# Optimization experiments

Hardware: AMD Instinct MI355X
Metric: run time of the kernel (lower is better)

Reference implementation:

```python
import jax, jax.numpy as jnp
import numpy as np

H = 768
NH = 12
DH = H // NH  # 64


def setup_inputs() -> dict:
    key = jax.random.key(0)
    ks = jax.random.split(key, 20)
    s = 1.0 / np.sqrt(H)
    def lin(k, din, dout):
        kw, kb = jax.random.split(k)
        W = jax.random.uniform(kw, (din, dout), jnp.float32, -s, s)
        b = jax.random.uniform(kb, (dout,), jnp.float32, -s, s)
        return W, b
    Wq, bq = lin(ks[0], H, H)
    Wk, bk = lin(ks[1], H, H)
    Wv, bv = lin(ks[2], H, H)
    Wt, bt = lin(ks[3], H, H)
    Wi, bi = lin(ks[4], H, H)
    W1, b1 = lin(ks[5], H, H)
    W2, b2 = lin(ks[6], H, 1)
    text = jax.random.normal(ks[7], (8, 64, H), jnp.float32)
    image = jax.random.normal(ks[8], (8, 197, H), jnp.float32)
    return dict(text=text, image=image, Wq=Wq, bq=bq, Wk=Wk, bk=bk, Wv=Wv, bv=bv,
                Wt=Wt, bt=bt, Wi=Wi, bi=bi, W1=W1, b1=b1, W2=W2, b2=b2)


def reference(text, image, Wq, bq, Wk, bk, Wv, bv, Wt, bt, Wi, bi, W1, b1, W2, b2):
    bsz, t_len, _ = text.shape
    i_len = image.shape[1]
    # relevance gate MLP on broadcast product
    text_emb = text @ Wt + bt          # [b, t, H]
    image_emb = image @ Wi + bi        # [b, i, H]
    rel = text_emb[:, :, None, :] * image_emb[:, None, :, :]  # [b, t, i, H]
    rel = jax.nn.relu(rel @ W1 + b1)
    gate = jax.nn.sigmoid(rel @ W2 + b2)  # [b, t, i, 1]
    gate = gate.reshape(bsz, 1, t_len, i_len)
    # cross-attention
    def heads(x, L):
        return x.reshape(bsz, L, NH, DH).transpose(0, 2, 1, 3)  # [b, h, L, dh]
    q = heads(text @ Wq + bq, t_len)
    k = heads(image @ Wk + bk, i_len)
    v = heads(image @ Wv + bv, i_len)
    scores = jnp.einsum('bhtd,bhid->bhti', q, k) / np.sqrt(DH)
    probs = jax.nn.softmax(scores, axis=-1) * gate   # [b, h, t, i]
    ctx = jnp.einsum('bhti,bhid->bhtd', probs, v)    # [b, h, t, dh]
    return ctx.transpose(0, 2, 1, 3).reshape(bsz, t_len, H)
```

## Files before the change

kernel.cpp:

```cpp
#include <hip/hip_runtime.h>
#include <stdint.h>

#define HD 768
#define NHEADS 12
#define DHEAD 64
#define BATCH 8
#define TLEN 64
#define ILEN 197
#define NPAIRS 100864
#define MTILES 394

typedef __attribute__((ext_vector_type(8))) short short8;
typedef __attribute__((ext_vector_type(4))) float f32x4;

__device__ __forceinline__ short f2bf(float x) {
    union { float f; uint32_t u; } v; v.f = x;
    uint32_t r = v.u + 0x7FFFu + ((v.u >> 16) & 1u);
    return (short)(r >> 16);
}
__device__ __forceinline__ float bf2f(short s) {
    union { uint32_t u; float f; } v; v.u = ((uint32_t)(unsigned short)s) << 16;
    return v.f;
}
__device__ __forceinline__ void gll16(const void* g, void* l) {
    __builtin_amdgcn_global_load_lds(
        (const __attribute__((address_space(1))) unsigned int*)g,
        (__attribute__((address_space(3))) unsigned int*)l, 16, 0, 0);
}

__global__ __launch_bounds__(256) void prep_weights(
    const float* __restrict__ Wq, const float* __restrict__ Wk,
    const float* __restrict__ Wv, const float* __restrict__ Wt,
    const float* __restrict__ Wi, const float* __restrict__ W1,
    short* __restrict__ W5s, short* __restrict__ W1Bs)
{
    __shared__ float tile[64][65];
    int bx = blockIdx.x;
    int tid = threadIdx.x;
    if (bx >= 720) {
        int idx = bx - 720;
        int pn = idx / 12, kt = idx - pn * 12;
        int c = tid;
        int j = pn * 256 + c;
        char* dst = (char*)W1Bs + (size_t)idx * 32768 + c * 128;
        int swz = (c & 7) << 4;
#pragma unroll
        for (int kg = 0; kg < 8; ++kg) {
            short8 o;
#pragma unroll
            for (int e = 0; e < 8; ++e)
                o[e] = f2bf(W1[(size_t)(kt * 64 + kg * 8 + e) * HD + j]);
            *(short8*)(dst + ((kg * 16) ^ swz)) = o;
        }
        return;
    }
    int seg = bx / 144, ti = bx - seg * 144;
    const float* src = (seg == 0) ? Wt : (seg == 1) ? Wq : (seg == 2) ? Wi
                     : (seg == 3) ? Wk : Wv;
    int kt = ti / 12, ntile = ti - kt * 12;
#pragma unroll
    for (int pass = 0; pass < 16; ++pass) {
        int idx = pass * 256 + tid;
        int kk = idx >> 6, nn = idx & 63;
        tile[kk][nn] = src[(size_t)(kt * 64 + kk) * HD + ntile * 64 + nn];
    }
    __syncthreads();
    size_t base = ((size_t)(seg * 12 + ntile) * 12 + kt) * 8192;
#pragma unroll
    for (int pass = 0; pass < 16; ++pass) {
        int idx = pass * 256 + tid;
        int col = idx >> 6, kloc = idx & 63;
        float x = tile[kloc][col];
        short h = f2bf(x);
        short lw = f2bf(x - bf2f(h));
        int sidx = (col * 64 + kloc) ^ ((col & 7) << 3);
        W5s[base + sidx] = h;
        W5s[base + 4096 + sidx] = lw;
    }
}

__global__ __launch_bounds__(256, 1) void proj_kernel(
    const float* __restrict__ X, int M,
    const short* __restrict__ W5s, int segbase,
    const float* __restrict__ bias0, const float* __restrict__ bias1,
    const float* __restrict__ bias2,
    float* __restrict__ out0, float* __restrict__ out1, float* __restrict__ out2)
{
    __shared__ __align__(16) short Bs[2][8192];
    int tid = threadIdx.x;
    int l = tid & 63, w = tid >> 6;
    int lo = l & 15, grp = l >> 4;
    int y = blockIdx.y;
    int segl = y / 12, ntile = y - segl * 12;
    int seg = segbase + segl;
    const char* wsrc = (const char*)W5s + (size_t)((seg * 12 + ntile) * 12) * 16384;
    {
        const char* s = wsrc + w * 4096 + l * 16;
        char* d = (char*)&Bs[0][0] + w * 4096;
        gll16(s, d); gll16(s + 1024, d + 1024);
        gll16(s + 2048, d + 2048); gll16(s + 3072, d + 3072);
    }
    int arow = blockIdx.x * 64 + w * 16 + lo;
    bool aok = arow < M;
    const float* xrow = X + (size_t)(aok ? arow : 0) * HD;
    short8 ah[24], al[24];
#pragma unroll
    for (int kc = 0; kc < 24; ++kc) {
        int kb = kc * 32 + grp * 8;
        float4 xa = {0.f, 0.f, 0.f, 0.f}, xb = {0.f, 0.f, 0.f, 0.f};
        if (aok) { xa = *(const float4*)(xrow + kb); xb = *(const float4*)(xrow + kb + 4); }
        float xs[8] = {xa.x, xa.y, xa.z, xa.w, xb.x, xb.y, xb.z, xb.w};
#pragma unroll
        for (int e = 0; e < 8; ++e) {
            short hh = f2bf(xs[e]);
            ah[kc][e] = hh;
            al[kc][e] = f2bf(xs[e] - bf2f(hh));
        }
    }
    __syncthreads();

    f32x4 acc[4];
    f32x4 z4 = {0.f, 0.f, 0.f, 0.f};
#pragma unroll
    for (int js = 0; js < 4; ++js) acc[js] = z4;

#pragma unroll
    for (int kk = 0; kk < 12; ++kk) {
        const short* buf = &Bs[kk & 1][0];
        if (kk < 11) {
            const char* s = wsrc + (size_t)(kk + 1) * 16384 + w * 4096 + l * 16;
            char* d = (char*)&Bs[(kk + 1) & 1][0] + w * 4096;
            gll16(s, d); gll16(s + 1024, d + 1024);
            gll16(s + 2048, d + 2048); gll16(s + 3072, d + 3072);
            asm volatile("s_waitcnt vmcnt(4)" ::: "memory");
        } else {
            asm volatile("s_waitcnt vmcnt(0)" ::: "memory");
        }
        __builtin_amdgcn_s_barrier();
        asm volatile("" ::: "memory");
#pragma unroll
        for (int js = 0; js < 4; ++js) {
            int col = js * 16 + lo;
            int base = col * 64;
            int sw = (col & 7) << 3;
#pragma unroll
            for (int kcl = 0; kcl < 2; ++kcl) {
                int idx = (base + kcl * 32 + grp * 8) ^ sw;
                short8 bh = *(const short8*)&buf[idx];
                short8 bl = *(const short8*)&buf[4096 + idx];
                int kc = kk * 2 + kcl;
                acc[js] = __builtin_amdgcn_mfma_f32_16x16x32_bf16(ah[kc], bh, acc[js], 0, 0, 0);
                acc[js] = __builtin_amdgcn_mfma_f32_16x16x32_bf16(ah[kc], bl, acc[js], 0, 0, 0);
                acc[js] = __builtin_amdgcn_mfma_f32_16x16x32_bf16(al[kc], bh, acc[js], 0, 0, 0);
            }
        }
        asm volatile("s_waitcnt lgkmcnt(0)" ::: "memory");
        __builtin_amdgcn_s_barrier();
        asm volatile("" ::: "memory");
    }
    const float* bp = (segl == 0) ? bias0 : (segl == 1) ? bias1 : bias2;
    float* op = (segl == 0) ? out0 : (segl == 1) ? out1 : out2;
#pragma unroll
    for (int js = 0; js < 4; ++js) {
        int cc = ntile * 64 + js * 16 + lo;
        float bvv = bp[cc];
#pragma unroll
        for (int r = 0; r < 4; ++r) {
            int orow = blockIdx.x * 64 + w * 16 + grp * 4 + r;
            if (orow < M) op[(size_t)orow * HD + cc] = acc[js][r] + bvv;
        }
    }
}

__global__ __launch_bounds__(256) void build_a(
    const float* __restrict__ te, const float* __restrict__ ie,
    short* __restrict__ As, int mstart)
{
    int bx = blockIdx.x;
    int m_l = bx / 12, kt = bx - m_l * 12;
    int tid = threadIdx.x;
    int p = (mstart + m_l) * 256 + tid;
    int b = p / 12608; int rr = p - b * 12608;
    int t = rr / 197;  int i = rr - t * 197;
    const float* tp = te + (size_t)(b * 64 + t) * HD + kt * 64;
    const float* ip = ie + (size_t)(b * 197 + i) * HD + kt * 64;
    char* dst = (char*)As + ((size_t)(m_l * 12 + kt) * 32768) + tid * 128;
    int swz = (tid & 7) << 4;
#pragma unroll
    for (int kg = 0; kg < 8; ++kg) {
        float4 xa = *(const float4*)(ip + kg * 8);
        float4 xb = *(const float4*)(ip + kg * 8 + 4);
        float4 ta = *(const float4*)(tp + kg * 8);
        float4 tb = *(const float4*)(tp + kg * 8 + 4);
        short8 o;
        o[0] = f2bf(xa.x * ta.x); o[1] = f2bf(xa.y * ta.y);
        o[2] = f2bf(xa.z * ta.z); o[3] = f2bf(xa.w * ta.w);
        o[4] = f2bf(xb.x * tb.x); o[5] = f2bf(xb.y * tb.y);
        o[6] = f2bf(xb.z * tb.z); o[7] = f2bf(xb.w * tb.w);
        *(short8*)(dst + ((kg * 16) ^ swz)) = o;
    }
}

__global__ __launch_bounds__(512, 2) void gate_gemm(
    const short* __restrict__ As, const short* __restrict__ W1Bs,
    const float* __restrict__ b1, const float* __restrict__ W2,
    float* __restrict__ plg, int mstart)
{
    __shared__ __align__(16) char lds[131072];
    int tid = threadIdx.x;
    int lane = tid & 63, wid = tid >> 6;
    int lo = lane & 15, grp = lane >> 4;
    int wr = wid >> 2, wc = wid & 3;
    int bx = blockIdx.x;
    int m_l = bx / 3, pn = bx - m_l * 3;

    const char* Ag = (const char*)As + (size_t)m_l * 12 * 32768;
    const char* Bg = (const char*)W1Bs + (size_t)pn * 12 * 32768;

    {
        gll16(Ag + tid * 16,          lds + tid * 16);
        gll16(Ag + 8192 + tid * 16,   lds + 8192 + tid * 16);
        gll16(Ag + 16384 + tid * 16,  lds + 16384 + tid * 16);
        gll16(Ag + 24576 + tid * 16,  lds + 24576 + tid * 16);
        gll16(Bg + tid * 16,          lds + 65536 + tid * 16);
        gll16(Bg + 8192 + tid * 16,   lds + 65536 + 8192 + tid * 16);
        gll16(Bg + 16384 + tid * 16,  lds + 65536 + 16384 + tid * 16);
        gll16(Bg + 24576 + tid * 16,  lds + 65536 + 24576 + tid * 16);
    }

    f32x4 acc[8][4];
    f32x4 z4 = {0.f, 0.f, 0.f, 0.f};
#pragma unroll
    for (int rt = 0; rt < 8; ++rt)
#pragma unroll
        for (int ct = 0; ct < 4; ++ct) acc[rt][ct] = z4;
    int swz = (lo & 7) << 4;

    for (int kt = 0; kt < 12; ++kt) {
        int par = kt & 1, npar = par ^ 1;
        int aoff = par * 32768;
        int boff = 65536 + par * 32768;
        const char* Aun = Ag + (size_t)(kt + 1) * 32768;
        const char* Bun = Bg + (size_t)(kt + 1) * 32768;
        bool more = kt < 11;
        short8 bfr[4][2];
#pragma unroll
        for (int q = 0; q < 4; ++q) {
            if (q == 0) {
                asm volatile("s_waitcnt vmcnt(0)" ::: "memory");
                __builtin_amdgcn_s_barrier();
                asm volatile("" ::: "memory");
            }
            if (more) {
                const char* s; int d;
                if (q < 2) { s = Aun + q * 16384; d = npar * 32768 + q * 16384; }
                else       { s = Bun + (q - 2) * 16384; d = 65536 + npar * 32768 + (q - 2) * 16384; }
                gll16(s + tid * 16, lds + d + tid * 16);
                gll16(s + 8192 + tid * 16, lds + d + 8192 + tid * 16);
            }
            if (q == 0) {
#pragma unroll
                for (int ct = 0; ct < 4; ++ct) {
                    int c = wc * 64 + ct * 16 + lo;
#pragma unroll
                    for (int ks = 0; ks < 2; ++ks)
                        bfr[ct][ks] = *(const short8*)(lds + boff + c * 128 + ((ks * 64 + grp * 16) ^ swz));
                }
            }
            short8 af[2][2];
#pragma unroll
            for (int i2 = 0; i2 < 2; ++i2) {
                int r = wr * 128 + (2 * q + i2) * 16 + lo;
#pragma unroll
                for (int ks = 0; ks < 2; ++ks)
                    af[i2][ks] = *(const short8*)(lds + aoff + r * 128 + ((ks * 64 + grp * 16) ^ swz));
            }
            __builtin_amdgcn_s_setprio(1);
#pragma unroll
            for (int i2 = 0; i2 < 2; ++i2)
#pragma unroll
                for (int ct = 0; ct < 4; ++ct)
#pragma unroll
                    for (int ks = 0; ks < 2; ++ks)
                        acc[2 * q + i2][ct] = __builtin_amdgcn_mfma_f32_16x16x32_bf16(
                            af[i2][ks], bfr[ct][ks], acc[2 * q + i2][ct], 0, 0, 0);
            __builtin_amdgcn_s_setprio(0);
            __builtin_amdgcn_s_barrier();
            asm volatile("" ::: "memory");
        }
    }

    float b1v[4], w2v[4];
#pragma unroll
    for (int ct = 0; ct < 4; ++ct) {
        int j = pn * 256 + wc * 64 + ct * 16 + lo;
        b1v[ct] = b1[j]; w2v[ct] = W2[j];
    }
    float pl[8][4];
#pragma unroll
    for (int rt = 0; rt < 8; ++rt)
#pragma unroll
        for (int r = 0; r < 4; ++r) {
            float s = 0.f;
#pragma unroll
            for (int ct = 0; ct < 4; ++ct)
                s += fmaxf(acc[rt][ct][r] + b1v[ct], 0.f) * w2v[ct];
            pl[rt][r] = s;
        }
#pragma unroll
    for (int msk = 1; msk <= 8; msk <<= 1)
#pragma unroll
        for (int rt = 0; rt < 8; ++rt)
#pragma unroll
            for (int r = 0; r < 4; ++r)
                pl[rt][r] += __shfl_xor(pl[rt][r], msk);

    __syncthreads();
    float* red = (float*)lds;
    if (lo == 0) {
#pragma unroll
        for (int rt = 0; rt < 8; ++rt)
#pragma unroll
            for (int r = 0; r < 4; ++r)
                red[wid * 128 + rt * 16 + grp * 4 + r] = pl[rt][r];
    }
    __syncthreads();
    if (tid < 256) {
        int wr_ = tid >> 7, rl = tid & 127;
        float s = red[(wr_ * 4 + 0) * 128 + rl] + red[(wr_ * 4 + 1) * 128 + rl]
                + red[(wr_ * 4 + 2) * 128 + rl] + red[(wr_ * 4 + 3) * 128 + rl];
        plg[(size_t)pn * NPAIRS + (size_t)(mstart + m_l) * 256 + tid] = s;
    }
}

__global__ __launch_bounds__(256) void gate_fin(
    const float* __restrict__ plg, const float* __restrict__ b2,
    float* __restrict__ gateb)
{
    int idx = blockIdx.x * 256 + threadIdx.x;
    if (idx < NPAIRS) {
        float s = plg[idx] + plg[NPAIRS + idx] + plg[2 * NPAIRS + idx] + b2[0];
        gateb[idx] = 1.f / (1.f + __expf(-s));
    }
}

__global__ __launch_bounds__(256) void attn_kernel(
    const float* __restrict__ q, const float* __restrict__ k,
    const float* __restrict__ v, const float* __restrict__ gate,
    float* __restrict__ out)
{
    __shared__ float k_s[ILEN * 65];
    __shared__ float p_s[4][200];
    int bx = blockIdx.x;
    int tq = bx & 3;
    int h = (bx >> 2) % NHEADS;
    int b = bx / (4 * NHEADS);
    int tid = threadIdx.x;
    for (int idx = tid; idx < ILEN * DHEAD; idx += 256) {
        int i = idx >> 6, d = idx & 63;
        k_s[i * 65 + d] = k[(size_t)(b * ILEN + i) * HD + h * DHEAD + d];
    }
    __syncthreads();

    int l = tid & 63, w = tid >> 6;
    for (int tt = 0; tt < 4; ++tt) {
        int t = tq * 16 + w * 4 + tt;
        float qv = q[(size_t)(b * 64 + t) * HD + h * DHEAD + l];
        float s0 = 0.f, s1 = 0.f, s2 = 0.f, s3 = 0.f;
        int i0 = l, i1 = 64 + l, i2 = 128 + l;
        int i3c = (192 + l < ILEN) ? 192 + l : 0;
        for (int d = 0; d < 64; ++d) {
            float qd = __shfl(qv, d);
            s0 += qd * k_s[i0 * 65 + d];
            s1 += qd * k_s[i1 * 65 + d];
            s2 += qd * k_s[i2 * 65 + d];
            s3 += qd * k_s[i3c * 65 + d];
        }
        float sc[4] = {s0, s1, s2, s3};
        float m = -3.0e38f;
#pragma unroll
        for (int rep = 0; rep < 4; ++rep) {
            int i = rep * 64 + l;
            sc[rep] = (i < ILEN) ? sc[rep] * 0.125f : -3.0e38f;
            m = fmaxf(m, sc[rep]);
        }
        for (int mask = 32; mask >= 1; mask >>= 1) m = fmaxf(m, __shfl_xor(m, mask));
        float sum = 0.f;
#pragma unroll
        for (int rep = 0; rep < 4; ++rep) {
            float e = __expf(sc[rep] - m);
            sc[rep] = e;
            sum += e;
        }
        for (int mask = 32; mask >= 1; mask >>= 1) sum += __shfl_xor(sum, mask);
        float inv = 1.f / sum;
        const float* grow = gate + (size_t)(b * 64 + t) * ILEN;
#pragma unroll
        for (int rep = 0; rep < 4; ++rep) {
            int i = rep * 64 + l;
            if (i < 200) p_s[w][i] = (i < ILEN) ? sc[rep] * inv * grow[i] : 0.f;
        }
        float ctx = 0.f;
        const float* vbase = v + (size_t)(b * ILEN) * HD + h * DHEAD + l;
        for (int c = 0; c < 49; ++c) {
            float4 p4 = *(const float4*)&p_s[w][c * 4];
            ctx += p4.x * vbase[(size_t)(c * 4 + 0) * HD];
            ctx += p4.y * vbase[(size_t)(c * 4 + 1) * HD];
            ctx += p4.z * vbase[(size_t)(c * 4 + 2) * HD];
            ctx += p4.w * vbase[(size_t)(c * 4 + 3) * HD];
        }
        {
            float4 p4 = *(const float4*)&p_s[w][196];
            ctx += p4.x * vbase[(size_t)196 * HD];
        }
        out[(size_t)(b * 64 + t) * HD + h * DHEAD + l] = ctx;
    }
}

extern "C" void kernel_launch(void* const* d_in, const int* in_sizes, int n_in,
                              void* d_out, int out_size, void* d_ws, size_t ws_size,
                              hipStream_t stream)
{
    const float* text  = (const float*)d_in[0];
    const float* image = (const float*)d_in[1];
    const float* Wq = (const float*)d_in[2];
    const float* bq = (const float*)d_in[3];
    const float* Wk = (const float*)d_in[4];
    const float* bk = (const float*)d_in[5];
    const float* Wv = (const float*)d_in[6];
    const float* bv = (const float*)d_in[7];
    const float* Wt = (const float*)d_in[8];
    const float* bt = (const float*)d_in[9];
    const float* Wi = (const float*)d_in[10];
    const float* bi = (const float*)d_in[11];
    const float* W1 = (const float*)d_in[12];
    const float* b1 = (const float*)d_in[13];
    const float* W2 = (const float*)d_in[14];
    const float* b2 = (const float*)d_in[15];
    float* out = (float*)d_out;

    char* ws = (char*)d_ws;
    size_t off = 0;
    auto carve = [&](size_t bytes) -> void* {
        void* p = (void*)(ws + off);
        off += (bytes + 255) & ~(size_t)255;
        return p;
    };
    short* W5s  = (short*)carve((size_t)5 * 144 * 8192 * 2);
    short* W1Bs = (short*)carve((size_t)36 * 32768);
    float* te    = (float*)carve((size_t)512 * 768 * 4);
    float* qb    = (float*)carve((size_t)512 * 768 * 4);
    float* ieb   = (float*)carve((size_t)1576 * 768 * 4);
    float* kb    = (float*)carve((size_t)1576 * 768 * 4);
    float* vb    = (float*)carve((size_t)1576 * 768 * 4);
    float* gateb = (float*)carve((size_t)NPAIRS * 4);
    float* plg   = (float*)carve((size_t)3 * NPAIRS * 4);

    size_t per_m = (size_t)12 * 32768;
    size_t avail = (ws_size > off) ? (ws_size - off) : 0;
    int stripe = (int)(avail / per_m);
    if (stripe > MTILES) stripe = MTILES;
    if (stripe < 1) stripe = 1;
    short* As = (short*)(ws + off);
    int nst = (MTILES + stripe - 1) / stripe;

    hipLaunchKernelGGL(prep_weights, dim3(756), dim3(256), 0, stream,
                       Wq, Wk, Wv, Wt, Wi, W1, W5s, W1Bs);
    hipLaunchKernelGGL(proj_kernel, dim3(8, 24), dim3(256), 0, stream,
                       text, 512, W5s, 0, bt, bq, (const float*)nullptr,
                       te, qb, (float*)nullptr);
    hipLaunchKernelGGL(proj_kernel, dim3(25, 36), dim3(256), 0, stream,
                       image, 1576, W5s, 2, bi, bk, bv,
                       ieb, kb, vb);
    for (int s = 0; s < nst; ++s) {
        int m0 = s * stripe;
        int mc = (MTILES - m0 < stripe) ? (MTILES - m0) : stripe;
        hipLaunchKernelGGL(build_a, dim3(mc * 12), dim3(256), 0, stream,
                           te, ieb, As, m0);
        hipLaunchKernelGGL(gate_gemm, dim3(mc * 3), dim3(512), 0, stream,
                           As, W1Bs, b1, W2, plg, m0);
    }
    hipLaunchKernelGGL(gate_fin, dim3((NPAIRS + 255) / 256), dim3(256), 0, stream,
                       plg, b2, gateb);
    hipLaunchKernelGGL(attn_kernel, dim3(BATCH * NHEADS * 4), dim3(256), 0, stream,
                       qb, kb, vb, gateb, out);
}
```

Measured before the change: 404.5 us.

## Remap blocks per XCD and batch prefetch loads with one barrier per k-step

Reorders workgroup-to-tile mapping so consecutive logical tiles run on the same XCD, aiming for better L2 reuse of shared A/B tiles. Restructures the k-loop to issue all next-stage global-to-LDS loads at once after a single barrier, removing the per-quarter barriers. This cuts synchronisation overhead but bunches memory traffic, which may reduce overlap with MFMA work.

```diff
diff --git a/kernel.cpp b/kernel.cpp
--- a/kernel.cpp
+++ b/kernel.cpp
@@ -210,9 +210,15 @@
     int tid = threadIdx.x;
     int lane = tid & 63, wid = tid >> 6;
     int lo = lane & 15, grp = lane >> 4;
-    int wr = wid >> 2, wc = wid & 3;
-    int bx = blockIdx.x;
-    int m_l = bx / 3, pn = bx - m_l * 3;
+    int wr = wid >> 2, wc = wid & 2 ? (wid & 3) : (wid & 3);
+    wc = wid & 3;
+    int bx0 = blockIdx.x;
+    int nwg = gridDim.x;
+    int qq = nwg >> 3, rr8 = nwg & 7;
+    int xcd = bx0 & 7;
+    int logical = (xcd < rr8 ? xcd * (qq + 1) : rr8 * (qq + 1) + (xcd - rr8) * qq)
+                + (bx0 >> 3);
+    int m_l = logical / 3, pn = logical - m_l * 3;
 
     const char* Ag = (const char*)As + (size_t)m_l * 12 * 32768;
     const char* Bg = (const char*)W1Bs + (size_t)pn * 12 * 32768;
@@ -240,33 +246,36 @@
         int par = kt & 1, npar = par ^ 1;
         int aoff = par * 32768;
         int boff = 65536 + par * 32768;
-        const char* Aun = Ag + (size_t)(kt + 1) * 32768;
-        const char* Bun = Bg + (size_t)(kt + 1) * 32768;
         bool more = kt < 11;
+
+        asm volatile("s_waitcnt vmcnt(0)" ::: "memory");
+        __builtin_amdgcn_s_barrier();
+        asm volatile("" ::: "memory");
+
+        if (more) {
+            const char* Aun = Ag + (size_t)(kt + 1) * 32768;
+            const char* Bun = Bg + (size_t)(kt + 1) * 32768;
+            int dA = npar * 32768, dB = 65536 + npar * 32768;
+            gll16(Aun + tid * 16,          lds + dA + tid * 16);
+            gll16(Aun + 8192 + tid * 16,   lds + dA + 8192 + tid * 16);
+            gll16(Aun + 16384 + tid * 16,  lds + dA + 16384 + tid * 16);
+            gll16(Aun + 24576 + tid * 16,  lds + dA + 24576 + tid * 16);
+            gll16(Bun + tid * 16,          lds + dB + tid * 16);
+            gll16(Bun + 8192 + tid * 16,   lds + dB + 8192 + tid * 16);
+            gll16(Bun + 16384 + tid * 16,  lds + dB + 16384 + tid * 16);
+            gll16(Bun + 24576 + tid * 16,  lds + dB + 24576 + tid * 16);
+        }
+
         short8 bfr[4][2];
 #pragma unroll
+        for (int ct = 0; ct < 4; ++ct) {
+            int c = wc * 64 + ct * 16 + lo;
+#pragma unroll
+            for (int ks = 0; ks < 2; ++ks)
+                bfr[ct][ks] = *(const short8*)(lds + boff + c * 128 + ((ks * 64 + grp * 16) ^ swz));
+        }
+#pragma unroll
         for (int q = 0; q < 4; ++q) {
-            if (q == 0) {
-                asm volatile("s_waitcnt vmcnt(0)" ::: "memory");
-                __builtin_amdgcn_s_barrier();
-                asm volatile("" ::: "memory");
-            }
-            if (more) {
-                const char* s; int d;
-                if (q < 2) { s = Aun + q * 16384; d = npar * 32768 + q * 16384; }
-                else       { s = Bun + (q - 2) * 16384; d = 65536 + npar * 32768 + (q - 2) * 16384; }
-                gll16(s + tid * 16, lds + d + tid * 16);
-                gll16(s + 8192 + tid * 16, lds + d + 8192 + tid * 16);
-            }
-            if (q == 0) {
-#pragma unroll
-                for (int ct = 0; ct < 4; ++ct) {
-                    int c = wc * 64 + ct * 16 + lo;
-#pragma unroll
-                    for (int ks = 0; ks < 2; ++ks)
-                        bfr[ct][ks] = *(const short8*)(lds + boff + c * 128 + ((ks * 64 + grp * 16) ^ swz));
-                }
-            }
             short8 af[2][2];
 #pragma unroll
             for (int i2 = 0; i2 < 2; ++i2) {
@@ -285,8 +294,6 @@
                         acc[2 * q + i2][ct] = __builtin_amdgcn_mfma_f32_16x16x32_bf16(
                             af[i2][ks], bfr[ct][ks], acc[2 * q + i2][ct], 0, 0, 0);
             __builtin_amdgcn_s_setprio(0);
-            __builtin_amdgcn_s_barrier();
-            asm volatile("" ::: "memory");
         }
     }
 
```

Result: faster. 389.1 us (-3.8%).
